# Kernel optimization log

Hardware: AMD Instinct MI355X
Metric: run time of the kernel (lower is better)

The kernel has to match this reference:

```python
import jax, jax.numpy as jnp
import numpy as np

C = 128
H, W, Z = 128, 128, 16
N_CLASSES = 20


def conv3d(x, w, b, padding='SAME'):
    # x: [B,C,D,H,W], w: [O,I,kd,kh,kw]
    y = jax.lax.conv_general_dilated(x, w, (1, 1, 1), padding,
                                     dimension_numbers=('NCDHW', 'OIDHW', 'NCDHW'))
    return y + b[None, :, None, None, None]


def setup_inputs() -> dict:
    key = jax.random.key(0)
    ks = jax.random.split(key, 16)
    s = lambda fan: 1.0 / np.sqrt(fan)
    inp = {}
    inp['x3d'] = jax.random.normal(ks[0], (1, C, H, W, Z), jnp.float32)
    inp['prob_3d'] = jax.random.uniform(ks[1], (1, 1, H, W, Z), jnp.float32)
    # bottleneck Conv3d(C, C, k=3, pad=1)
    inp['w_bot'] = jax.random.normal(ks[2], (C, C, 3, 3, 3), jnp.float32) * s(C * 27)
    inp['b_bot'] = jnp.zeros((C,), jnp.float32)
    # occ_header: SDB(C -> C//2) approximated as conv3x3 + leaky_relu, then Conv3d(C//2, 2, k=3)
    inp['w_occ1'] = jax.random.normal(ks[3], (C // 2, C, 3, 3, 3), jnp.float32) * s(C * 27)
    inp['b_occ1'] = jnp.zeros((C // 2,), jnp.float32)
    inp['w_occ2'] = jax.random.normal(ks[4], (2, C // 2, 3, 3, 3), jnp.float32) * s(C // 2 * 27)
    inp['b_occ2'] = jnp.zeros((2,), jnp.float32)
    # mlp_prior: Linear(C, C//2) -> LayerNorm -> LeakyReLU -> Linear(C//2, C)
    inp['w_mlp1'] = jax.random.normal(ks[5], (C, C // 2), jnp.float32) * s(C)
    inp['b_mlp1'] = jnp.zeros((C // 2,), jnp.float32)
    inp['ln_g'] = jnp.ones((C // 2,), jnp.float32)
    inp['ln_b'] = jnp.zeros((C // 2,), jnp.float32)
    inp['w_mlp2'] = jax.random.normal(ks[6], (C // 2, C), jnp.float32) * s(C // 2)
    inp['b_mlp2'] = jnp.zeros((C,), jnp.float32)
    # sdb: Conv3d(C, C//2, k=3) + leaky_relu
    inp['w_sdb'] = jax.random.normal(ks[7], (C // 2, C, 3, 3, 3), jnp.float32) * s(C * 27)
    inp['b_sdb'] = jnp.zeros((C // 2,), jnp.float32)
    # ssc_header: Conv3d(C//2, n_classes, k=1)
    inp['w_ssc'] = jax.random.normal(ks[8], (N_CLASSES, C // 2, 1, 1, 1), jnp.float32) * s(C // 2)
    inp['b_ssc'] = jnp.zeros((N_CLASSES,), jnp.float32)
    return inp


def reference(x3d, prob_3d, w_bot, b_bot, w_occ1, b_occ1, w_occ2, b_occ2,
              w_mlp1, b_mlp1, ln_g, ln_b, w_mlp2, b_mlp2, w_sdb, b_sdb,
              w_ssc, b_ssc):
    # dense 3D bottleneck conv
    x = conv3d(x3d, w_bot, b_bot)  # [1,C,H,W,Z]
    # occupancy head on depth-reweighted features
    occ_in = x * prob_3d + x
    occ_h = jax.nn.leaky_relu(conv3d(occ_in, w_occ1, b_occ1))
    occ_logit = conv3d(occ_h, w_occ2, b_occ2)  # [1,2,H,W,Z]
    occ_prob = jax.nn.softmax(occ_logit, axis=1)[:, 1]  # [1,H,W,Z]
    occ_mask = (occ_prob > 0.5).reshape(-1)  # [N]

    # flatten voxel features: [N, C]
    x_flat = x[0].reshape(C, -1).T
    # prior MLP for non-occupied voxels (LayerNorm over feature dim)
    h = x_flat @ w_mlp1 + b_mlp1
    mu = jnp.mean(h, axis=-1, keepdims=True)
    var = jnp.var(h, axis=-1, keepdims=True)
    h = (h - mu) / jnp.sqrt(var + 1e-5) * ln_g + ln_b
    h = jax.nn.leaky_relu(h)
    prior = h @ w_mlp2 + b_mlp2  # [N, C]

    # gather/scatter fused as a masked select:
    # occupied voxels keep seed features, empty voxels take the prior
    vox_flat = jnp.where(occ_mask[:, None], x_flat, prior)  # [N, C]
    vox = vox_flat.T.reshape(1, C, H, W, Z)

    # SDB diffusion conv + SSC head
    d = jax.nn.leaky_relu(conv3d(vox, w_sdb, b_sdb))  # [1,C//2,H,W,Z]
    ssc_logit = conv3d(d, w_ssc, b_ssc)  # [1,20,H,W,Z]
    return ssc_logit
```

## Files before the change

### kernel.cpp

```cpp
#include <hip/hip_runtime.h>

#define AD 128
#define BDW 128
#define ZD 16
#define NVOX (AD*BDW*ZD)
#define SLAB 32768
#define NSLAB 8

typedef __attribute__((ext_vector_type(4))) float f32x4;
typedef __attribute__((ext_vector_type(8))) short bf16x8;
typedef __attribute__((ext_vector_type(8))) short s16x8;

__device__ __forceinline__ float leaky(float v) { return v > 0.f ? v : 0.01f * v; }

__device__ __forceinline__ f32x4 mfma16(bf16x8 a, bf16x8 b, f32x4 c) {
    return __builtin_amdgcn_mfma_f32_16x16x32_bf16(a, b, c, 0, 0, 0);
}

__device__ __forceinline__ void split3(float v, unsigned short& s1,
                                       unsigned short& s2, unsigned short& s3) {
    const unsigned u1 = __float_as_uint(v) & 0xFFFF0000u;
    const float r1 = v - __uint_as_float(u1);
    const unsigned u2 = __float_as_uint(r1) & 0xFFFF0000u;
    const float r2 = r1 - __uint_as_float(u2);
    s1 = (unsigned short)(u1 >> 16);
    s2 = (unsigned short)(u2 >> 16);
    s3 = (unsigned short)(__float_as_uint(r2) >> 16);
}

__device__ __forceinline__ int lds_a_off(int v, int chunk) {
    return ((v << 5) + (chunk << 3)) ^ ((v & 7) << 3);
}

__global__ __launch_bounds__(256) void wsplit3(const float* __restrict__ w,
                                               unsigned short* __restrict__ wp, int OC) {
    const int i = blockIdx.x * 256 + threadIdx.x;
    const int PS = OC * 3456;
    if (i >= PS) return;
    const int ko = i & 7;
    const int oc = (i >> 3) % OC;
    const int rest = (i >> 3) / OC;
    const int kc = rest & 3;
    const int kbt = rest >> 2;
    const int kb = kbt & 3, t = kbt >> 2;
    const int ic = kb * 32 + kc * 8 + ko;
    const float v = w[((size_t)oc * 128 + ic) * 27 + t];
    unsigned short s1, s2, s3;
    split3(v, s1, s2, s3);
    wp[i] = s1; wp[i + PS] = s2; wp[i + 2 * PS] = s3;
}

template<int OC, int PROD, bool PREMUL, bool LEAKY, int RING, bool FUSESSC>
__global__ __launch_bounds__(256, 2) void conv3s(const float* __restrict__ src,
                                              const float* __restrict__ prob,
                                              const unsigned short* __restrict__ W,
                                              const float* __restrict__ bias,
                                              float* __restrict__ out,
                                              const float* __restrict__ wssc,
                                              const float* __restrict__ bssc,
                                              int ablk_base) {
    constexpr int NPL = (PROD == 6) ? 3 : 2;
    constexpr int PLH = 324 * 32;
    __shared__ __align__(16) unsigned short smraw[NPL * PLH];
    unsigned short* sm0 = smraw;
    unsigned short* sm1 = smraw + PLH;
    unsigned short* sm2 = smraw + (NPL - 1) * PLH;

    const int tid = threadIdx.x;
    const int cpx = gridDim.x >> 3;
    const int bx = (blockIdx.x & 7) * cpx + (blockIdx.x >> 3);

    const int ablk = ablk_base + (bx >> 5);
    const int b0   = (bx & 31) * 4;
    const int vblock = ablk * 2048 + b0 * 16;

    const int w = tid >> 6, l = tid & 63;
    const int lo16 = l & 15, hi4 = l >> 4;
    constexpr int NF = OC / 64;
    constexpr int PS = OC * 3456;
    const int oc_off = w * (16 * NF);

    f32x4 acc[4][NF];
    #pragma unroll
    for (int nf = 0; nf < NF; ++nf) {
        const float bv = bias[oc_off + nf * 16 + lo16];
        #pragma unroll
        for (int mf = 0; mf < 4; ++mf) acc[mf][nf] = f32x4{bv, bv, bv, bv};
    }

    float pf[6][8];
    float pfpm[6];

    #define PREFETCH(KB)                                                          \
        _Pragma("unroll")                                                         \
        for (int it = 0; it < 6; ++it) {                                          \
            const int i = tid + it * 256;                                         \
            _Pragma("unroll")                                                     \
            for (int j = 0; j < 8; ++j) pf[it][j] = 0.f;                          \
            pfpm[it] = 1.f;                                                       \
            if (i < 1296) {                                                       \
                const int q8 = i / 324;                                           \
                const int v  = i - q8 * 324;                                      \
                const int col = v / 18;                                           \
                const int zz  = v - col * 18;                                     \
                const int ta  = col / 6;                                          \
                const int bi  = col - ta * 6;                                     \
                const int a = ablk + ta - 1;                                      \
                const int b = b0 + bi - 1;                                        \
                const int z = zz - 1;                                             \
                if (((unsigned)a < 128u) && ((unsigned)b < 128u) &&               \
                    ((unsigned)z < 16u)) {                                        \
                    const int q = a * 2048 + b * 16 + z;                          \
                    const float* sp = src + (size_t)((KB) * 32 + q8 * 8) * NVOX + q; \
                    _Pragma("unroll")                                             \
                    for (int j = 0; j < 8; ++j) pf[it][j] = sp[(size_t)j * NVOX]; \
                    if (PREMUL) pfpm[it] = 1.f + prob[q];                         \
                }                                                                 \
            }                                                                     \
        }

    PREFETCH(0)

    #pragma unroll 1
    for (int kb = 0; kb < 4; ++kb) {
        __syncthreads();
        #pragma unroll
        for (int it = 0; it < 6; ++it) {
            const int i = tid + it * 256;
            if (i < 1296) {
                const int q8 = i / 324;
                const int v  = i - q8 * 324;
                s16x8 t1, t2, t3;
                #pragma unroll
                for (int j = 0; j < 8; ++j) {
                    float f = pf[it][j];
                    if (PREMUL) f *= pfpm[it];
                    unsigned short s1, s2, s3;
                    split3(f, s1, s2, s3);
                    t1[j] = (short)s1; t2[j] = (short)s2; t3[j] = (short)s3;
                }
                const int off = lds_a_off(v, q8);
                *(s16x8*)(sm0 + off) = t1;
                *(s16x8*)(sm1 + off) = t2;
                if (NPL == 3) *(s16x8*)(sm2 + off) = t3;
            }
        }
        if (kb < 3) PREFETCH(kb + 1)
        __syncthreads();

        #pragma unroll 1
        for (int ta = 0; ta < 3; ++ta) {
            #pragma unroll 1
            for (int tz = 0; tz < 3; ++tz) {
                bf16x8 A1[6], A2[6], A3[6];
                #pragma unroll
                for (int s = 0; s < 6; ++s) {
                    const int v = (ta * 6 + s) * 18 + lo16 + tz;
                    const int ao = lds_a_off(v, hi4);
                    A1[s] = *(const bf16x8*)(sm0 + ao);
                    A2[s] = *(const bf16x8*)(sm1 + ao);
                    if (PROD == 6) A3[s] = *(const bf16x8*)(sm2 + ao);
                }
                #pragma unroll
                for (int tb = 0; tb < 3; ++tb) {
                    const int t = ta * 9 + tb * 3 + tz;
                    bf16x8 b1[NF], b2[NF], b3[NF];
                    #pragma unroll
                    for (int nf = 0; nf < NF; ++nf) {
                        const size_t wb = (((size_t)(t * 4 + kb) * 4 + hi4) * OC
                                           + oc_off + nf * 16 + lo16) * 8;
                        b1[nf] = *(const bf16x8*)(W + wb);
                        b2[nf] = *(const bf16x8*)(W + PS + wb);
                        if (PROD == 6) b3[nf] = *(const bf16x8*)(W + 2 * PS + wb);
                    }
                    #pragma unroll
                    for (int mf = 0; mf < 4; ++mf) {
                        const int s = mf + tb;
                        #pragma unroll
                        for (int nf = 0; nf < NF; ++nf) {
                            acc[mf][nf] = mfma16(A1[s], b1[nf], acc[mf][nf]);
                            acc[mf][nf] = mfma16(A1[s], b2[nf], acc[mf][nf]);
                            acc[mf][nf] = mfma16(A2[s], b1[nf], acc[mf][nf]);
                        }
                        if (PROD == 6) {
                            #pragma unroll
                            for (int nf = 0; nf < NF; ++nf) {
                                acc[mf][nf] = mfma16(A2[s], b2[nf], acc[mf][nf]);
                                acc[mf][nf] = mfma16(A1[s], b3[nf], acc[mf][nf]);
                                acc[mf][nf] = mfma16(A3[s], b1[nf], acc[mf][nf]);
                            }
                        }
                    }
                }
            }
        }
    }
    #undef PREFETCH

    __syncthreads();
    float* ldsT = (float*)smraw;
    #pragma unroll
    for (int mf = 0; mf < 4; ++mf)
        #pragma unroll
        for (int nf = 0; nf < NF; ++nf) {
            const int oc = oc_off + nf * 16 + lo16;
            #pragma unroll
            for (int r = 0; r < 4; ++r) {
                float vv = acc[mf][nf][r];
                if (LEAKY) vv = leaky(vv);
                ldsT[oc * 65 + mf * 16 + hi4 * 4 + r] = vv;
            }
        }
    __syncthreads();
    if (FUSESSC) {
        for (int i = tid; i < 20 * 64; i += 256) {
            const int v = i & 63;
            const int o = i >> 6;
            float acc2 = bssc[o];
            #pragma unroll
            for (int ic = 0; ic < 64; ++ic)
                acc2 = fmaf(ldsT[ic * 65 + v], wssc[o * 64 + ic], acc2);
            out[(size_t)o * NVOX + vblock + v] = acc2;
        }
    } else {
        int ocol;
        if (RING == 0) ocol = vblock;
        else           ocol = ((ablk >> 4) % 3) * SLAB + (vblock & (SLAB - 1));
        const size_t outN = (RING == 0) ? (size_t)NVOX : (size_t)(3 * SLAB);
        for (int i = tid; i < OC * 64; i += 256) {
            const int oc = i >> 6, v = i & 63;
            out[(size_t)oc * outN + ocol + v] = ldsT[oc * 65 + v];
        }
    }
}

__global__ __launch_bounds__(256, 2) void occ2s(const float* __restrict__ HR,
                                                const float* __restrict__ w,
                                                const float* __restrict__ bias,
                                                unsigned char* __restrict__ mask,
                                                int s) {
    __shared__ float hl[324 * 36];
    __shared__ float wl[3456];
    __shared__ float red0[4][66], red1[4][66];

    const int tid = threadIdx.x;
    for (int i = tid; i < 3456; i += 256) wl[i] = w[i];

    const int p0 = s * SLAB + blockIdx.x * 64;
    const int a0r = p0 >> 11;
    const int bb0 = (p0 >> 4) & 127;
    const int g = tid >> 6, v64 = tid & 63;

    float a0 = 0.f, a1 = 0.f;
    #pragma unroll 1
    for (int half = 0; half < 2; ++half) {
        __syncthreads();
        for (int i = tid; i < 2592; i += 256) {
            const int q4 = i / 324;
            const int v  = i - q4 * 324;
            const int col = v / 18;
            const int zz  = v - col * 18;
            const int ta  = col / 6;
            const int bi  = col - ta * 6;
            const int a = a0r + ta - 1;
            const int b = bb0 + bi - 1;
            const int z = zz - 1;
            f32x4 val = {0.f, 0.f, 0.f, 0.f};
            if (((unsigned)a < 128u) && ((unsigned)b < 128u) && ((unsigned)z < 16u)) {
                const int q = a * 2048 + b * 16 + z;
                const int rc = ((a >> 4) % 3) * SLAB + (q & (SLAB - 1));
                const int ic0 = half * 32 + q4 * 4;
                #pragma unroll
                for (int j = 0; j < 4; ++j)
                    val[j] = HR[(size_t)(ic0 + j) * (3 * SLAB) + rc];
            }
            *(f32x4*)(hl + v * 36 + q4 * 4) = val;
        }
        __syncthreads();
        #pragma unroll 1
        for (int t = 0; t < 27; ++t) {
            const int ta = t / 9, tb = (t / 3) % 3, tz = t % 3;
            const int vt = (ta * 6 + (v64 >> 4) + tb) * 18 + (v64 & 15) + tz;
            #pragma unroll
            for (int j = 0; j < 8; ++j) {
                const int icl = g * 8 + j;
                const int ic = half * 32 + icl;
                const float hh = hl[vt * 36 + icl];
                a0 = fmaf(hh, wl[ic * 27 + t], a0);
                a1 = fmaf(hh, wl[1728 + ic * 27 + t], a1);
            }
        }
    }
    red0[g][v64] = a0; red1[g][v64] = a1;
    __syncthreads();
    if (g == 0) {
        float t0 = bias[0], t1 = bias[1];
        #pragma unroll
        for (int k = 0; k < 4; ++k) { t0 += red0[k][v64]; t1 += red1[k][v64]; }
        mask[p0 + v64] = (t1 > t0) ? 1 : 0;
    }
}

__global__ __launch_bounds__(256) void mlp_vox(float* __restrict__ x,
                                               const float* __restrict__ w1,
                                               const float* __restrict__ b1,
                                               const float* __restrict__ g,
                                               const float* __restrict__ beta,
                                               const float* __restrict__ w2,
                                               const float* __restrict__ b2,
                                               const unsigned char* __restrict__ mask) {
    const int p = blockIdx.x * 256 + threadIdx.x;
    float h[64];
    #pragma unroll
    for (int j = 0; j < 64; ++j) h[j] = b1[j];
    #pragma unroll 1
    for (int c = 0; c < 128; ++c) {
        const float xv = x[(size_t)c * NVOX + p];
        #pragma unroll
        for (int j = 0; j < 64; ++j) h[j] = fmaf(xv, w1[c * 64 + j], h[j]);
    }
    float mu = 0.f;
    #pragma unroll
    for (int j = 0; j < 64; ++j) mu += h[j];
    mu *= (1.f / 64.f);
    float var = 0.f;
    #pragma unroll
    for (int j = 0; j < 64; ++j) { const float d = h[j] - mu; var = fmaf(d, d, var); }
    var *= (1.f / 64.f);
    const float rs = rsqrtf(var + 1e-5f);
    #pragma unroll
    for (int j = 0; j < 64; ++j) h[j] = leaky((h[j] - mu) * rs * g[j] + beta[j]);

    const bool m = mask[p] != 0;
    #pragma unroll 1
    for (int c = 0; c < 128; ++c) {
        float pr = b2[c];
        #pragma unroll
        for (int j = 0; j < 64; ++j) pr = fmaf(h[j], w2[j * 128 + c], pr);
        const size_t idx = (size_t)c * NVOX + p;
        x[idx] = m ? x[idx] : pr;
    }
}

extern "C" void kernel_launch(void* const* d_in, const int* in_sizes, int n_in,
                              void* d_out, int out_size, void* d_ws, size_t ws_size,
                              hipStream_t stream) {
    const float* x3d    = (const float*)d_in[0];
    const float* prob   = (const float*)d_in[1];
    const float* w_bot  = (const float*)d_in[2];
    const float* b_bot  = (const float*)d_in[3];
    const float* w_occ1 = (const float*)d_in[4];
    const float* b_occ1 = (const float*)d_in[5];
    const float* w_occ2 = (const float*)d_in[6];
    const float* b_occ2 = (const float*)d_in[7];
    const float* w_mlp1 = (const float*)d_in[8];
    const float* b_mlp1 = (const float*)d_in[9];
    const float* ln_g   = (const float*)d_in[10];
    const float* ln_b   = (const float*)d_in[11];
    const float* w_mlp2 = (const float*)d_in[12];
    const float* b_mlp2 = (const float*)d_in[13];
    const float* w_sdb  = (const float*)d_in[14];
    const float* b_sdb  = (const float*)d_in[15];
    const float* w_ssc  = (const float*)d_in[16];
    const float* b_ssc  = (const float*)d_in[17];

    char* ws = (char*)d_ws;
    float* X32 = (float*)(ws);
    float* HR  = (float*)(ws + 134217728);
    unsigned short* WB3 = (unsigned short*)(ws + 159383552);
    unsigned short* W13 = (unsigned short*)(ws + 162037760);
    unsigned short* WS3 = (unsigned short*)(ws + 163364864);
    unsigned char* mask = (unsigned char*)(ws + 164691968);

    const dim3 blk(256);

    wsplit3<<<1728, blk, 0, stream>>>(w_bot,  WB3, 128);
    wsplit3<<<864,  blk, 0, stream>>>(w_occ1, W13, 64);
    wsplit3<<<864,  blk, 0, stream>>>(w_sdb,  WS3, 64);

    conv3s<128, 6, false, false, 0, false><<<4096, blk, 0, stream>>>(
        x3d, nullptr, WB3, b_bot, X32, nullptr, nullptr, 0);

    for (int s = 0; s < NSLAB; ++s) {
        conv3s<64, 6, true, true, 2, false><<<512, blk, 0, stream>>>(
            X32, prob, W13, b_occ1, HR, nullptr, nullptr, 16 * s);
        if (s >= 1) occ2s<<<512, blk, 0, stream>>>(HR, w_occ2, b_occ2, mask, s - 1);
    }
    occ2s<<<512, blk, 0, stream>>>(HR, w_occ2, b_occ2, mask, NSLAB - 1);

    mlp_vox<<<1024, blk, 0, stream>>>(X32, w_mlp1, b_mlp1, ln_g, ln_b, w_mlp2, b_mlp2, mask);

    conv3s<64, 3, false, true, 0, true><<<4096, blk, 0, stream>>>(
        X32, nullptr, WS3, b_sdb, (float*)d_out, w_ssc, b_ssc, 0);
}
```

Measured before the change: 2.421 ms.

## Double conv3 block tile along A with 512-thread blocks sharing halo

```diff
diff --git a/kernel.cpp b/kernel.cpp
--- a/kernel.cpp
+++ b/kernel.cpp
@@ -51,7 +51,7 @@
 }
 
 template<int OC, int PROD, bool PREMUL, bool LEAKY, int RING, bool FUSESSC>
-__global__ __launch_bounds__(256, 2) void conv3s(const float* __restrict__ src,
+__global__ __launch_bounds__(512, 1) void conv3s(const float* __restrict__ src,
                                               const float* __restrict__ prob,
                                               const unsigned short* __restrict__ W,
                                               const float* __restrict__ bias,
@@ -60,7 +60,7 @@
                                               const float* __restrict__ bssc,
                                               int ablk_base) {
     constexpr int NPL = (PROD == 6) ? 3 : 2;
-    constexpr int PLH = 324 * 32;
+    constexpr int PLH = 432 * 32;
     __shared__ __align__(16) unsigned short smraw[NPL * PLH];
     unsigned short* sm0 = smraw;
     unsigned short* sm1 = smraw + PLH;
@@ -70,15 +70,16 @@
     const int cpx = gridDim.x >> 3;
     const int bx = (blockIdx.x & 7) * cpx + (blockIdx.x >> 3);
 
-    const int ablk = ablk_base + (bx >> 5);
-    const int b0   = (bx & 31) * 4;
-    const int vblock = ablk * 2048 + b0 * 16;
+    const int ablk2 = ablk_base + (bx >> 5);
+    const int b0    = (bx & 31) * 4;
+    const int vbase = ablk2 * 4096 + b0 * 16;
 
     const int w = tid >> 6, l = tid & 63;
     const int lo16 = l & 15, hi4 = l >> 4;
+    const int wo = w & 3, wm = w >> 2;
     constexpr int NF = OC / 64;
     constexpr int PS = OC * 3456;
-    const int oc_off = w * (16 * NF);
+    const int oc_off = wo * (16 * NF);
 
     f32x4 acc[4][NF];
     #pragma unroll
@@ -88,25 +89,25 @@
         for (int mf = 0; mf < 4; ++mf) acc[mf][nf] = f32x4{bv, bv, bv, bv};
     }
 
-    float pf[6][8];
-    float pfpm[6];
+    float pf[4][8];
+    float pfpm[4];
 
     #define PREFETCH(KB)                                                          \
         _Pragma("unroll")                                                         \
-        for (int it = 0; it < 6; ++it) {                                          \
-            const int i = tid + it * 256;                                         \
+        for (int it = 0; it < 4; ++it) {                                          \
+            const int i = tid + it * 512;                                         \
             _Pragma("unroll")                                                     \
             for (int j = 0; j < 8; ++j) pf[it][j] = 0.f;                          \
             pfpm[it] = 1.f;                                                       \
-            if (i < 1296) {                                                       \
-                const int q8 = i / 324;                                           \
-                const int v  = i - q8 * 324;                                      \
+            if (i < 1728) {                                                       \
+                const int q8 = i / 432;                                           \
+                const int v  = i - q8 * 432;                                      \
                 const int col = v / 18;                                           \
                 const int zz  = v - col * 18;                                     \
-                const int ta  = col / 6;                                          \
-                const int bi  = col - ta * 6;                                     \
-                const int a = ablk + ta - 1;                                      \
-                const int b = b0 + bi - 1;                                        \
+                const int ha  = col / 6;                                          \
+                const int hb  = col - ha * 6;                                     \
+                const int a = ablk2 * 2 + ha - 1;                                 \
+                const int b = b0 + hb - 1;                                        \
                 const int z = zz - 1;                                             \
                 if (((unsigned)a < 128u) && ((unsigned)b < 128u) &&               \
                     ((unsigned)z < 16u)) {                                        \
@@ -125,11 +126,11 @@
     for (int kb = 0; kb < 4; ++kb) {
         __syncthreads();
         #pragma unroll
-        for (int it = 0; it < 6; ++it) {
-            const int i = tid + it * 256;
-            if (i < 1296) {
-                const int q8 = i / 324;
-                const int v  = i - q8 * 324;
+        for (int it = 0; it < 4; ++it) {
+            const int i = tid + it * 512;
+            if (i < 1728) {
+                const int q8 = i / 432;
+                const int v  = i - q8 * 432;
                 s16x8 t1, t2, t3;
                 #pragma unroll
                 for (int j = 0; j < 8; ++j) {
@@ -155,7 +156,7 @@
                 bf16x8 A1[6], A2[6], A3[6];
                 #pragma unroll
                 for (int s = 0; s < 6; ++s) {
-                    const int v = (ta * 6 + s) * 18 + lo16 + tz;
+                    const int v = ((wm + ta) * 6 + s) * 18 + lo16 + tz;
                     const int ao = lds_a_off(v, hi4);
                     A1[s] = *(const bf16x8*)(sm0 + ao);
                     A2[s] = *(const bf16x8*)(sm1 + ao);
@@ -208,28 +209,29 @@
             for (int r = 0; r < 4; ++r) {
                 float vv = acc[mf][nf][r];
                 if (LEAKY) vv = leaky(vv);
-                ldsT[oc * 65 + mf * 16 + hi4 * 4 + r] = vv;
+                ldsT[oc * 129 + wm * 64 + mf * 16 + hi4 * 4 + r] = vv;
             }
         }
     __syncthreads();
     if (FUSESSC) {
-        for (int i = tid; i < 20 * 64; i += 256) {
-            const int v = i & 63;
-            const int o = i >> 6;
+        for (int i = tid; i < 20 * 128; i += 512) {
+            const int tv = i & 127;
+            const int o = i >> 7;
             float acc2 = bssc[o];
             #pragma unroll
             for (int ic = 0; ic < 64; ++ic)
-                acc2 = fmaf(ldsT[ic * 65 + v], wssc[o * 64 + ic], acc2);
-            out[(size_t)o * NVOX + vblock + v] = acc2;
+                acc2 = fmaf(ldsT[ic * 129 + tv], wssc[o * 64 + ic], acc2);
+            out[(size_t)o * NVOX + vbase + (tv >> 6) * 2048 + (tv & 63)] = acc2;
         }
     } else {
-        int ocol;
-        if (RING == 0) ocol = vblock;
-        else           ocol = ((ablk >> 4) % 3) * SLAB + (vblock & (SLAB - 1));
+        int obase;
+        if (RING == 0) obase = vbase;
+        else           obase = ((ablk2 >> 3) % 3) * SLAB + (vbase & (SLAB - 1));
         const size_t outN = (RING == 0) ? (size_t)NVOX : (size_t)(3 * SLAB);
-        for (int i = tid; i < OC * 64; i += 256) {
-            const int oc = i >> 6, v = i & 63;
-            out[(size_t)oc * outN + ocol + v] = ldsT[oc * 65 + v];
+        for (int i = tid; i < OC * 128; i += 512) {
+            const int oc = i >> 7, tv = i & 127;
+            out[(size_t)oc * outN + obase + (tv >> 6) * 2048 + (tv & 63)] =
+                ldsT[oc * 129 + tv];
         }
     }
 }
@@ -373,23 +375,24 @@
     unsigned char* mask = (unsigned char*)(ws + 164691968);
 
     const dim3 blk(256);
+    const dim3 blk5(512);
 
     wsplit3<<<1728, blk, 0, stream>>>(w_bot,  WB3, 128);
     wsplit3<<<864,  blk, 0, stream>>>(w_occ1, W13, 64);
     wsplit3<<<864,  blk, 0, stream>>>(w_sdb,  WS3, 64);
 
-    conv3s<128, 6, false, false, 0, false><<<4096, blk, 0, stream>>>(
+    conv3s<128, 6, false, false, 0, false><<<2048, blk5, 0, stream>>>(
         x3d, nullptr, WB3, b_bot, X32, nullptr, nullptr, 0);
 
     for (int s = 0; s < NSLAB; ++s) {
-        conv3s<64, 6, true, true, 2, false><<<512, blk, 0, stream>>>(
-            X32, prob, W13, b_occ1, HR, nullptr, nullptr, 16 * s);
+        conv3s<64, 6, true, true, 2, false><<<256, blk5, 0, stream>>>(
+            X32, prob, W13, b_occ1, HR, nullptr, nullptr, 8 * s);
         if (s >= 1) occ2s<<<512, blk, 0, stream>>>(HR, w_occ2, b_occ2, mask, s - 1);
     }
     occ2s<<<512, blk, 0, stream>>>(HR, w_occ2, b_occ2, mask, NSLAB - 1);
 
     mlp_vox<<<1024, blk, 0, stream>>>(X32, w_mlp1, b_mlp1, ln_g, ln_b, w_mlp2, b_mlp2, mask);
 
-    conv3s<64, 3, false, true, 0, true><<<4096, blk, 0, stream>>>(
+    conv3s<64, 3, false, true, 0, true><<<2048, blk5, 0, stream>>>(
         X32, nullptr, WS3, b_sdb, (float*)d_out, w_ssc, b_ssc, 0);
 }
```

Result: no change. 2.390 ms (-1.3%).
